# Kernel tuning notes

Measured on AMD Instinct MI355X. Metric: run time of the kernel, lower is better.

## Reference

```python
import jax, jax.numpy as jnp
import numpy as np

NUM_HEADS = 16
HEAD_DIM = 64  # hidden 1024 / 16


def setup_inputs() -> dict:
    key = jax.random.key(0)
    k1, k2, k3 = jax.random.split(key, 3)
    B, S, H = 2, 2048, 1024
    return {
        "hidden_states": jax.random.normal(k1, (B, S, H), dtype=jnp.float32),
        "attention_mask": jnp.zeros((B, 1, 1, S), dtype=jnp.float32),
        "c_attn_w": jax.random.normal(k2, (H, 3 * H), dtype=jnp.float32) * 0.02,
        "c_attn_b": jnp.zeros((3 * H,), dtype=jnp.float32),
        "c_proj_w": jax.random.normal(k3, (H, H), dtype=jnp.float32) * 0.02,
        "c_proj_b": jnp.zeros((H,), dtype=jnp.float32),
    }


def reference(hidden_states, attention_mask, c_attn_w, c_attn_b, c_proj_w, c_proj_b):
    B, S, H = hidden_states.shape
    nH, hd = NUM_HEADS, HEAD_DIM
    # Conv1D: x @ w + b (HF weight layout is (in, out))
    qkv = hidden_states @ c_attn_w + c_attn_b  # [B,S,3H]
    q, k, v = jnp.split(qkv, 3, axis=-1)
    # split heads -> [B,nH,S,hd]
    def heads(t):
        return t.reshape(B, S, nH, hd).transpose(0, 2, 1, 3)
    q, k, v = heads(q), heads(k), heads(v)
    scores = jnp.einsum("bhqd,bhkd->bhqk", q, k) / np.sqrt(hd).astype(jnp.float32)
    scores = scores + attention_mask  # additive mask, broadcast [B,1,1,S]
    attn = jax.nn.softmax(scores, axis=-1)  # dropout is identity (eval)
    ctx = jnp.einsum("bhqk,bhkd->bhqd", attn, v)
    ctx = ctx.transpose(0, 2, 1, 3).reshape(B, S, H)  # merge heads
    out = ctx @ c_proj_w + c_proj_b
    return out
```

## Files before the change

### kernel.cpp

```cpp
#include <hip/hip_runtime.h>
#include <hip/hip_bf16.h>

typedef __attribute__((ext_vector_type(8))) short short8;
typedef __attribute__((ext_vector_type(4))) short short4v;
typedef __attribute__((ext_vector_type(4))) float f32x4;

__device__ __forceinline__ unsigned short f2bf(float f) {
  union { __hip_bfloat16 h; unsigned short u; } cv;
  cv.h = __float2bfloat16(f);
  return cv.u;
}

__device__ __forceinline__ void gld16(const void* g, void* l) {
  __builtin_amdgcn_global_load_lds(
      (const __attribute__((address_space(1))) unsigned int*)g,
      (__attribute__((address_space(3))) unsigned int*)l, 16, 0, 0);
}

__device__ __forceinline__ f32x4 mfma_bf16(short8 a, short8 b, f32x4 c) {
  return __builtin_amdgcn_mfma_f32_16x16x32_bf16(a, b, c, 0, 0, 0);
}

#define QSCALE 0.18033688011112042f
#define L2E    1.4426950408889634f

__global__ void prep(const float* __restrict__ x, unsigned short* __restrict__ xbf,
                     const float* __restrict__ wa, unsigned short* __restrict__ da,
                     const float* __restrict__ wp, unsigned short* __restrict__ dp) {
  __shared__ float tile[64][65];
  const int t = threadIdx.x;
  const int bid = blockIdx.x;
  if (bid < 4096) {
    int i = bid * 256 + t;
    float4 v = ((const float4*)x)[i];
    ushort4 o;
    o.x = f2bf(v.x); o.y = f2bf(v.y); o.z = f2bf(v.z); o.w = f2bf(v.w);
    ((ushort4*)xbf)[i] = o;
    return;
  }
  int idx = bid - 4096;
  const int tr = idx & 15;
  int y = idx >> 4;
  const float* src;
  unsigned short* dst;
  int C;
  if (y < 48) { src = wa; dst = da; C = 3072; }
  else        { src = wp; dst = dp; C = 1024; y -= 48; }
  const int tc = y;
#pragma unroll
  for (int i = 0; i < 16; ++i) {
    int id2 = t + i * 256;
    int lr = id2 >> 6, lc = id2 & 63;
    tile[lr][lc] = src[(size_t)(tr * 64 + lr) * C + tc * 64 + lc];
  }
  __syncthreads();
#pragma unroll
  for (int i = 0; i < 16; ++i) {
    int id2 = t + i * 256;
    int lr = id2 >> 6, lc = id2 & 63;
    dst[(size_t)(tc * 64 + lr) * 1024 + tr * 64 + lc] = f2bf(tile[lc][lr]);
  }
}

template <int KDIM>
__device__ __forceinline__ void gemm_core(const short* __restrict__ A, const short* __restrict__ Bt,
                                          int mbase, int nbase, short* As, short* Bs,
                                          int wm, int wn, int quad, int l16, int t,
                                          f32x4 (&acc)[4][4]) {
  for (int kt = 0; kt < KDIM / 32; ++kt) {
#pragma unroll
    for (int i = 0; i < 2; ++i) {
      int c = t + i * 256;
      int row = c >> 2, c4 = c & 3;
      gld16(A + (size_t)(mbase + row) * KDIM + kt * 32 + c4 * 8, (char*)As + c * 16);
      gld16(Bt + (size_t)(nbase + row) * KDIM + kt * 32 + c4 * 8, (char*)Bs + c * 16);
    }
    __syncthreads();
    short8 af[4], bf[4];
#pragma unroll
    for (int m = 0; m < 4; ++m)
      af[m] = *(const short8*)((const char*)As + (wm + m * 16 + l16) * 64 + quad * 16);
#pragma unroll
    for (int n = 0; n < 4; ++n)
      bf[n] = *(const short8*)((const char*)Bs + (wn + n * 16 + l16) * 64 + quad * 16);
#pragma unroll
    for (int m = 0; m < 4; ++m)
#pragma unroll
      for (int n = 0; n < 4; ++n)
        acc[m][n] = mfma_bf16(af[m], bf[n], acc[m][n]);
    __syncthreads();
  }
}

__global__ __launch_bounds__(256, 2) void gemm_qkv(
    const short* __restrict__ A, const short* __restrict__ Bt, const float* __restrict__ bias,
    unsigned short* __restrict__ q, unsigned short* __restrict__ k,
    unsigned short* __restrict__ vt) {
  __shared__ __align__(16) char smem[17408];
  short* As = (short*)smem;
  short* Bs = (short*)(smem + 8192);
  unsigned short* vlds = (unsigned short*)smem;
  const int t = threadIdx.x;
  const int wave = t >> 6, lane = t & 63;
  const int quad = lane >> 4, l16 = lane & 15;
  const int wm = (wave >> 1) * 64, wn = (wave & 1) * 64;
  const int mbase = blockIdx.x * 128, nbase = blockIdx.y * 128;
  f32x4 acc[4][4];
#pragma unroll
  for (int i = 0; i < 4; ++i)
#pragma unroll
    for (int j = 0; j < 4; ++j) acc[i][j] = (f32x4)0.0f;
  gemm_core<1024>(A, Bt, mbase, nbase, As, Bs, wm, wn, quad, l16, t, acc);

  if (nbase < 2048) {
#pragma unroll
    for (int n = 0; n < 4; ++n) {
      int col = nbase + wn + n * 16 + l16;
      float bc = bias[col];
      int which = col >> 10, rem = col & 1023;
      int h = rem >> 6, d = rem & 63;
      unsigned short* dst = which ? k : q;
      float scale = which ? 1.0f : QSCALE;
#pragma unroll
      for (int m = 0; m < 4; ++m) {
#pragma unroll
        for (int r = 0; r < 4; ++r) {
          int row = mbase + wm + m * 16 + quad * 4 + r;
          int b = row >> 11, s = row & 2047;
          dst[(((size_t)(b * 16 + h)) * 2048 + s) * 64 + d] = f2bf((acc[m][n][r] + bc) * scale);
        }
      }
    }
  } else {
    const int b = mbase >> 11, s0 = mbase & 2047;
    const int vcb = nbase - 2048;
    __syncthreads();
#pragma unroll
    for (int half = 0; half < 2; ++half) {
      if (wn == half * 64) {
#pragma unroll
        for (int n = 0; n < 4; ++n) {
          int col_l = n * 16 + l16;
          float bc = bias[nbase + half * 64 + col_l];
#pragma unroll
          for (int m = 0; m < 4; ++m)
#pragma unroll
            for (int r = 0; r < 4; ++r) {
              int row_l = wm + m * 16 + quad * 4 + r;
              int idx = (row_l & 64) + (row_l & 15) * 4 + ((row_l >> 4) & 3);
              vlds[col_l * 136 + idx] = f2bf(acc[m][n][r] + bc);
            }
        }
      }
      __syncthreads();
      int h = (vcb + half * 64) >> 6;
      size_t obase = ((size_t)(b * 16 + h)) * 64 * 2048;
#pragma unroll
      for (int i = 0; i < 4; ++i) {
        int c = t + i * 256;
        int d_l = c >> 4, c16 = c & 15;
        short8 v = *(const short8*)&vlds[d_l * 136 + c16 * 8];
        *(short8*)&vt[obase + (size_t)d_l * 2048 + s0 + c16 * 8] = v;
      }
      __syncthreads();
    }
  }
}

__global__ __launch_bounds__(256, 2) void gemm_proj(
    const short* __restrict__ A, const short* __restrict__ Bt, const float* __restrict__ bias,
    float* __restrict__ out) {
  __shared__ __align__(16) short As[64 * 32];
  __shared__ __align__(16) short Bs[128 * 32];
  const int t = threadIdx.x;
  const int wave = t >> 6, lane = t & 63;
  const int quad = lane >> 4, l16 = lane & 15;
  const int wm = (wave >> 1) * 32, wn = (wave & 1) * 64;
  const int mbase = blockIdx.x * 64, nbase = blockIdx.y * 128;
  f32x4 acc[2][4];
#pragma unroll
  for (int i = 0; i < 2; ++i)
#pragma unroll
    for (int j = 0; j < 4; ++j) acc[i][j] = (f32x4)0.0f;
  for (int kt = 0; kt < 32; ++kt) {
    {
      int row = t >> 2, c4 = t & 3;
      gld16(A + (size_t)(mbase + row) * 1024 + kt * 32 + c4 * 8, (char*)As + t * 16);
    }
#pragma unroll
    for (int i = 0; i < 2; ++i) {
      int c = t + i * 256;
      int row = c >> 2, c4 = c & 3;
      gld16(Bt + (size_t)(nbase + row) * 1024 + kt * 32 + c4 * 8, (char*)Bs + c * 16);
    }
    __syncthreads();
    short8 af[2], bf[4];
#pragma unroll
    for (int m = 0; m < 2; ++m)
      af[m] = *(const short8*)((const char*)As + (wm + m * 16 + l16) * 64 + quad * 16);
#pragma unroll
    for (int n = 0; n < 4; ++n)
      bf[n] = *(const short8*)((const char*)Bs + (wn + n * 16 + l16) * 64 + quad * 16);
#pragma unroll
    for (int m = 0; m < 2; ++m)
#pragma unroll
      for (int n = 0; n < 4; ++n)
        acc[m][n] = mfma_bf16(af[m], bf[n], acc[m][n]);
    __syncthreads();
  }
#pragma unroll
  for (int n = 0; n < 4; ++n) {
    int col = nbase + wn + n * 16 + l16;
    float bc = bias[col];
#pragma unroll
    for (int m = 0; m < 2; ++m)
#pragma unroll
      for (int r = 0; r < 4; ++r) {
        int row = mbase + wm + m * 16 + quad * 4 + r;
        out[(size_t)row * 1024 + col] = acc[m][n][r] + bc;
      }
  }
}

__global__ __launch_bounds__(256, 2) void flash_attn(
    const short* __restrict__ Qg, const short* __restrict__ Kg, const short* __restrict__ Vtg,
    const float* __restrict__ mask, unsigned short* __restrict__ ctx) {
  __shared__ __align__(16) unsigned char smem[49152];
  short* Psm = (short*)(smem + 32768);
  const int t = threadIdx.x;
  const int wave = t >> 6, lane = t & 63;
  const int quad = lane >> 4, l16 = lane & 15;
  const int bh = blockIdx.x, b = bh >> 4, h = bh & 15;
  const int qbase = blockIdx.y * 128;
  const size_t bh_off = (size_t)bh * 2048 * 64;

#pragma unroll
  for (int i = 0; i < 4; ++i) {
    int c = t + i * 256;
    int row = c >> 3, col = c & 7;
    gld16(Qg + bh_off + (size_t)(qbase + row) * 64 + (col ^ (row & 7)) * 8,
          (char*)smem + c * 16);
  }
  __syncthreads();
  short8 qf[2][2];
#pragma unroll
  for (int mf = 0; mf < 2; ++mf)
#pragma unroll
    for (int ks = 0; ks < 2; ++ks) {
      int row = wave * 32 + mf * 16 + l16;
      qf[mf][ks] = *(const short8*)((const char*)smem +
                                    (row * 8 + ((ks * 4 + quad) ^ (l16 & 7))) * 16);
    }
  __syncthreads();

  auto stage = [&](int kn) {
    char* kd = (char*)smem + (kn & 1) * 8192;
    char* vd = (char*)smem + 16384 + (kn & 1) * 8192;
#pragma unroll
    for (int i = 0; i < 2; ++i) {
      int c = t + i * 256;
      int row = c >> 3, col = c & 7;
      gld16(Kg + bh_off + (size_t)(kn * 64 + row) * 64 + (col ^ (row & 7)) * 8,
            kd + c * 16);
      gld16(Vtg + ((size_t)bh * 64 + row) * 2048 + kn * 64 + (col ^ (row & 7)) * 8,
            vd + c * 16);
    }
  };

  f32x4 O[2][4];
  float l_i[2][4];
#pragma unroll
  for (int mf = 0; mf < 2; ++mf)
#pragma unroll
    for (int d = 0; d < 4; ++d) O[mf][d] = (f32x4)0.0f;
#pragma unroll
  for (int mf = 0; mf < 2; ++mf)
#pragma unroll
    for (int r = 0; r < 4; ++r) l_i[mf][r] = 0.0f;

  stage(0);
  __syncthreads();

  for (int kt = 0; kt < 32; ++kt) {
    const char* Kc = (const char*)smem + (kt & 1) * 8192;
    const char* Vc = (const char*)smem + 16384 + (kt & 1) * 8192;

    float mv[4];
#pragma unroll
    for (int n = 0; n < 4; ++n) mv[n] = mask[b * 2048 + kt * 64 + n * 16 + l16];

    if (kt < 31) stage(kt + 1);

    f32x4 sa[2][4];
#pragma unroll
    for (int mf = 0; mf < 2; ++mf)
#pragma unroll
      for (int n = 0; n < 4; ++n) sa[mf][n] = (f32x4)0.0f;
    __builtin_amdgcn_s_setprio(1);
#pragma unroll
    for (int ks = 0; ks < 2; ++ks) {
#pragma unroll
      for (int n = 0; n < 4; ++n) {
        int row = n * 16 + l16;
        short8 kf = *(const short8*)(Kc + (row * 8 + ((ks * 4 + quad) ^ (l16 & 7))) * 16);
        sa[0][n] = mfma_bf16(qf[0][ks], kf, sa[0][n]);
        sa[1][n] = mfma_bf16(qf[1][ks], kf, sa[1][n]);
      }
    }
    __builtin_amdgcn_s_setprio(0);

#pragma unroll
    for (int mf = 0; mf < 2; ++mf) {
#pragma unroll
      for (int r = 0; r < 4; ++r) {
        float rs = 0.0f;
        short4v p4;
#pragma unroll
        for (int n = 0; n < 4; ++n) {
          float p = __builtin_amdgcn_exp2f(__builtin_fmaf(mv[n], L2E, sa[mf][n][r]));
          rs += p;
          p4[n] = (short)f2bf(p);
        }
        int prow = wave * 32 + mf * 16 + quad * 4 + r;
        *(short4v*)((char*)Psm + prow * 128 +
                    (((l16 >> 1) ^ (prow & 7)) * 16) + (l16 & 1) * 8) = p4;
        l_i[mf][r] += rs;
      }
    }
    asm volatile("" ::: "memory");

    __builtin_amdgcn_s_setprio(1);
#pragma unroll
    for (int ks = 0; ks < 2; ++ks) {
      int u = ks * 4 + quad;
      short8 vf[4];
#pragma unroll
      for (int db = 0; db < 4; ++db) {
        int d = db * 16 + l16;
        vf[db] = *(const short8*)(Vc + d * 128 + ((u ^ (d & 7)) * 16));
      }
#pragma unroll
      for (int mf = 0; mf < 2; ++mf) {
        int prow = wave * 32 + mf * 16 + l16;
        short8 pf = *(const short8*)((const char*)Psm + prow * 128 + ((u ^ (l16 & 7)) * 16));
#pragma unroll
        for (int db = 0; db < 4; ++db)
          O[mf][db] = mfma_bf16(pf, vf[db], O[mf][db]);
      }
    }
    __builtin_amdgcn_s_setprio(0);

    __syncthreads();
  }

#pragma unroll
  for (int mf = 0; mf < 2; ++mf) {
#pragma unroll
    for (int r = 0; r < 4; ++r) {
      float l = l_i[mf][r];
      l += __shfl_xor(l, 1);
      l += __shfl_xor(l, 2);
      l += __shfl_xor(l, 4);
      l += __shfl_xor(l, 8);
      float inv = 1.0f / l;
      int s = qbase + wave * 32 + mf * 16 + quad * 4 + r;
      size_t o = ((size_t)b * 2048 + s) * 1024 + h * 64;
#pragma unroll
      for (int db = 0; db < 4; ++db)
        ctx[o + db * 16 + l16] = f2bf(O[mf][db][r] * inv);
    }
  }
}

extern "C" void kernel_launch(void* const* d_in, const int* in_sizes, int n_in,
                              void* d_out, int out_size, void* d_ws, size_t ws_size,
                              hipStream_t stream) {
  const float* x      = (const float*)d_in[0];
  const float* mask   = (const float*)d_in[1];
  const float* w_attn = (const float*)d_in[2];
  const float* b_attn = (const float*)d_in[3];
  const float* w_proj = (const float*)d_in[4];
  const float* b_proj = (const float*)d_in[5];
  float* out = (float*)d_out;

  char* ws = (char*)d_ws;
  const size_t MB = 1024 * 1024;
  short*          Xbf    = (short*)(ws);
  short*          Wqkv_t = (short*)(ws + 8 * MB);
  short*          Wprj_t = (short*)(ws + 14 * MB);
  unsigned short* Qb     = (unsigned short*)(ws + 16 * MB);
  unsigned short* Kb     = (unsigned short*)(ws + 24 * MB);
  unsigned short* Vtb    = (unsigned short*)(ws + 32 * MB);
  unsigned short* ctx    = (unsigned short*)Xbf;

  prep<<<5120, 256, 0, stream>>>(x, (unsigned short*)Xbf,
                                 w_attn, (unsigned short*)Wqkv_t,
                                 w_proj, (unsigned short*)Wprj_t);
  gemm_qkv<<<dim3(32, 24), 256, 0, stream>>>(Xbf, Wqkv_t, b_attn, Qb, Kb, Vtb);
  flash_attn<<<dim3(32, 16), 256, 0, stream>>>((const short*)Qb, (const short*)Kb,
                                               (const short*)Vtb, mask, ctx);
  gemm_proj<<<dim3(64, 8), 256, 0, stream>>>((const short*)ctx, Wprj_t, b_proj, out);
}
```

Baseline: 184.5 us.

## Keep softmax probabilities in registers by computing transposed S = K·Qᵀ

```diff
diff --git a/kernel.cpp b/kernel.cpp
--- a/kernel.cpp
+++ b/kernel.cpp
@@ -2,7 +2,6 @@
 #include <hip/hip_bf16.h>
 
 typedef __attribute__((ext_vector_type(8))) short short8;
-typedef __attribute__((ext_vector_type(4))) short short4v;
 typedef __attribute__((ext_vector_type(4))) float f32x4;
 
 __device__ __forceinline__ unsigned short f2bf(float f) {
@@ -147,7 +146,8 @@
 #pragma unroll
             for (int r = 0; r < 4; ++r) {
               int row_l = wm + m * 16 + quad * 4 + r;
-              int idx = (row_l & 64) + (row_l & 15) * 4 + ((row_l >> 4) & 3);
+              int idx = (row_l & 64) + ((row_l >> 5) & 1) * 32 +
+                        ((row_l >> 2) & 3) * 8 + ((row_l >> 4) & 1) * 4 + (row_l & 3);
               vlds[col_l * 136 + idx] = f2bf(acc[m][n][r] + bc);
             }
         }
@@ -225,8 +225,7 @@
 __global__ __launch_bounds__(256, 2) void flash_attn(
     const short* __restrict__ Qg, const short* __restrict__ Kg, const short* __restrict__ Vtg,
     const float* __restrict__ mask, unsigned short* __restrict__ ctx) {
-  __shared__ __align__(16) unsigned char smem[49152];
-  short* Psm = (short*)(smem + 32768);
+  __shared__ __align__(16) unsigned char smem[32768];
   const int t = threadIdx.x;
   const int wave = t >> 6, lane = t & 63;
   const int quad = lane >> 4, l16 = lane & 15;
@@ -268,15 +267,13 @@
   };
 
   f32x4 O[2][4];
-  float l_i[2][4];
+  float l_part[2];
 #pragma unroll
   for (int mf = 0; mf < 2; ++mf)
 #pragma unroll
     for (int d = 0; d < 4; ++d) O[mf][d] = (f32x4)0.0f;
-#pragma unroll
-  for (int mf = 0; mf < 2; ++mf)
-#pragma unroll
-    for (int r = 0; r < 4; ++r) l_i[mf][r] = 0.0f;
+  l_part[0] = 0.0f;
+  l_part[1] = 0.0f;
 
   stage(0);
   __syncthreads();
@@ -285,9 +282,10 @@
     const char* Kc = (const char*)smem + (kt & 1) * 8192;
     const char* Vc = (const char*)smem + 16384 + (kt & 1) * 8192;
 
-    float mv[4];
-#pragma unroll
-    for (int n = 0; n < 4; ++n) mv[n] = mask[b * 2048 + kt * 64 + n * 16 + l16];
+    float4 mq[4];
+#pragma unroll
+    for (int n = 0; n < 4; ++n)
+      mq[n] = *(const float4*)&mask[b * 2048 + kt * 64 + n * 16 + quad * 4];
 
     if (kt < 31) stage(kt + 1);
 
@@ -303,49 +301,38 @@
       for (int n = 0; n < 4; ++n) {
         int row = n * 16 + l16;
         short8 kf = *(const short8*)(Kc + (row * 8 + ((ks * 4 + quad) ^ (l16 & 7))) * 16);
-        sa[0][n] = mfma_bf16(qf[0][ks], kf, sa[0][n]);
-        sa[1][n] = mfma_bf16(qf[1][ks], kf, sa[1][n]);
+        sa[0][n] = mfma_bf16(kf, qf[0][ks], sa[0][n]);
+        sa[1][n] = mfma_bf16(kf, qf[1][ks], sa[1][n]);
       }
     }
     __builtin_amdgcn_s_setprio(0);
 
+    short8 pa[2][2];
 #pragma unroll
     for (int mf = 0; mf < 2; ++mf) {
-#pragma unroll
-      for (int r = 0; r < 4; ++r) {
-        float rs = 0.0f;
-        short4v p4;
-#pragma unroll
-        for (int n = 0; n < 4; ++n) {
-          float p = __builtin_amdgcn_exp2f(__builtin_fmaf(mv[n], L2E, sa[mf][n][r]));
+      float rs = 0.0f;
+#pragma unroll
+      for (int n = 0; n < 4; ++n) {
+#pragma unroll
+        for (int r = 0; r < 4; ++r) {
+          float p = __builtin_amdgcn_exp2f(__builtin_fmaf(mq[n][r], L2E, sa[mf][n][r]));
           rs += p;
-          p4[n] = (short)f2bf(p);
+          pa[mf][n >> 1][(n & 1) * 4 + r] = (short)f2bf(p);
         }
-        int prow = wave * 32 + mf * 16 + quad * 4 + r;
-        *(short4v*)((char*)Psm + prow * 128 +
-                    (((l16 >> 1) ^ (prow & 7)) * 16) + (l16 & 1) * 8) = p4;
-        l_i[mf][r] += rs;
-      }
-    }
-    asm volatile("" ::: "memory");
+      }
+      l_part[mf] += rs;
+    }
 
     __builtin_amdgcn_s_setprio(1);
 #pragma unroll
     for (int ks = 0; ks < 2; ++ks) {
       int u = ks * 4 + quad;
-      short8 vf[4];
 #pragma unroll
       for (int db = 0; db < 4; ++db) {
         int d = db * 16 + l16;
-        vf[db] = *(const short8*)(Vc + d * 128 + ((u ^ (d & 7)) * 16));
-      }
-#pragma unroll
-      for (int mf = 0; mf < 2; ++mf) {
-        int prow = wave * 32 + mf * 16 + l16;
-        short8 pf = *(const short8*)((const char*)Psm + prow * 128 + ((u ^ (l16 & 7)) * 16));
-#pragma unroll
-        for (int db = 0; db < 4; ++db)
-          O[mf][db] = mfma_bf16(pf, vf[db], O[mf][db]);
+        short8 vf = *(const short8*)(Vc + d * 128 + ((u ^ (d & 7)) * 16));
+        O[0][db] = mfma_bf16(pa[0][ks], vf, O[0][db]);
+        O[1][db] = mfma_bf16(pa[1][ks], vf, O[1][db]);
       }
     }
     __builtin_amdgcn_s_setprio(0);
@@ -353,16 +340,20 @@
     __syncthreads();
   }
 
+  float lr[2];
 #pragma unroll
   for (int mf = 0; mf < 2; ++mf) {
+    float l = l_part[mf];
+    l += __shfl_xor(l, 16);
+    l += __shfl_xor(l, 32);
+    lr[mf] = l;
+  }
+#pragma unroll
+  for (int mf = 0; mf < 2; ++mf) {
 #pragma unroll
     for (int r = 0; r < 4; ++r) {
-      float l = l_i[mf][r];
-      l += __shfl_xor(l, 1);
-      l += __shfl_xor(l, 2);
-      l += __shfl_xor(l, 4);
-      l += __shfl_xor(l, 8);
-      float inv = 1.0f / l;
+      float lq = __shfl(lr[mf], quad * 4 + r);
+      float inv = 1.0f / lq;
       int s = qbase + wave * 32 + mf * 16 + quad * 4 + r;
       size_t o = ((size_t)b * 2048 + s) * 1024 + h * 64;
 #pragma unroll
```

Result: faster. 177.4 us (-3.9%).
